# Kernel tuning notes

Measured on AMD Instinct MI355X. Metric: run time of the kernel, lower is better.

Reference implementation:

```python
import jax, jax.numpy as jnp
import numpy as np

B, T, F, H, C = 256, 14, 1024, 1024, 2513


def lstm_step(Wih, Whh, bih, bhh, x, h, c):
    # PyTorch LSTM cell: gate order i, f, g, o
    g = x @ Wih.T + bih + h @ Whh.T + bhh
    i, f, gg, o = jnp.split(g, 4, axis=-1)
    i = jax.nn.sigmoid(i)
    f = jax.nn.sigmoid(f)
    gg = jnp.tanh(gg)
    o = jax.nn.sigmoid(o)
    c = f * c + i * gg
    h = o * jnp.tanh(c)
    return h, c


def setup_inputs() -> dict:
    key = jax.random.key(0)
    ks = jax.random.split(key, 11)
    s = 1.0 / np.sqrt(H)
    u = lambda k, shape: jax.random.uniform(k, shape, jnp.float32, -s, s)
    return {
        "inputs": jax.random.normal(ks[0], (B, T, F), jnp.float32),
        "roll_Wih": u(ks[1], (4 * H, F)),
        "roll_Whh": u(ks[2], (4 * H, H)),
        "roll_bih": u(ks[3], (4 * H,)),
        "roll_bhh": u(ks[4], (4 * H,)),
        "unroll_Wih": u(ks[5], (4 * H, F)),
        "unroll_Whh": u(ks[6], (4 * H, H)),
        "unroll_bih": u(ks[7], (4 * H,)),
        "unroll_bhh": u(ks[8], (4 * H,)),
        "cls_W": u(ks[9], (C, H)),
        "cls_b": u(ks[10], (C,)),
    }


def reference(inputs, roll_Wih, roll_Whh, roll_bih, roll_bhh,
              unroll_Wih, unroll_Whh, unroll_bih, unroll_bhh, cls_W, cls_b):
    x_t = jnp.transpose(inputs, (1, 0, 2))  # [T, B, F]

    # Rolling LSTM: scan over time, keep hidden/cell at every step
    h0 = jnp.zeros((B, H), inputs.dtype)
    c0 = jnp.zeros((B, H), inputs.dtype)

    def roll(carry, xt):
        h, c = carry
        h, c = lstm_step(roll_Wih, roll_Whh, roll_bih, roll_bhh, xt, h, c)
        return (h, c), (h, c)

    _, (hs, cs) = jax.lax.scan(roll, (h0, c0), x_t)  # each [T, B, H]

    # Unrolling LSTM: for each t, feed inputs[t] repeated (T - t + 1) times,
    # starting from (hs[t], cs[t]). Vectorized over t: run T+1 steps for all
    # branches with constant per-branch input x_t[t], then pick step (T - t).
    def unroll(carry, _):
        h, c = carry  # [T, B, H]
        h, c = lstm_step(unroll_Wih, unroll_Whh, unroll_bih, unroll_bhh, x_t, h, c)
        return (h, c), h

    _, h_all = jax.lax.scan(unroll, (hs, cs), None, length=T + 1)  # [T+1, T, B, H]
    t_idx = jnp.arange(T)
    h_n = h_all[T - t_idx, t_idx]  # [T, B, H], last output of each branch

    x = jnp.transpose(h_n, (1, 0, 2))  # [B, T, H]
    y = x @ cls_W.T + cls_b  # [B, T, C]
    return y
```

## Files before the change

### kernel.cpp

```cpp
#include <hip/hip_runtime.h>

#define DEVFN __device__ __forceinline__

typedef __bf16 bf16x8 __attribute__((ext_vector_type(8)));
typedef float floatx4 __attribute__((ext_vector_type(4)));
typedef unsigned short us4 __attribute__((ext_vector_type(4)));


DEVFN unsigned short f2bf(float x) {
    union { float f; unsigned u; } v; v.f = x;
    v.u += 0x7FFFu + ((v.u >> 16) & 1u);
    return (unsigned short)(v.u >> 16);
}

DEVFN float bf2f(unsigned short s) {
    union { unsigned u; float f; } v; v.u = ((unsigned)s) << 16; return v.f;
}

DEVFN float sigm(float x) { return 1.f / (1.f + __expf(-x)); }
DEVFN float tanh_fast(float x) { float t = __expf(2.f * x); return 1.f - 2.f / (t + 1.f); }

DEVFN void gload_lds16(const unsigned short* g, unsigned short* l) {
    __builtin_amdgcn_global_load_lds(
        (__attribute__((address_space(1))) unsigned int*)g,
        (__attribute__((address_space(3))) unsigned int*)l, 16, 0, 0);
}

#define CFENCE asm volatile("" ::: "memory")


__global__ __launch_bounds__(256) void transpose_bt(const float* __restrict__ in,
                                                    unsigned short* __restrict__ out) {
    int idx = blockIdx.x * 256 + threadIdx.x;
    int k4 = (idx & 255) << 2;
    int row = idx >> 8;
    int t = row >> 8, b = row & 255;
    float4 v = *(const float4*)(in + (size_t)(b * 14 + t) * 1024 + k4);
    us4 o = {f2bf(v.x), f2bf(v.y), f2bf(v.z), f2bf(v.w)};
    *(us4*)(out + (size_t)row * 1024 + k4) = o;
}

__global__ __launch_bounds__(256) void conv_w4(const float* __restrict__ s0, const float* __restrict__ s1,
                                               const float* __restrict__ s2, const float* __restrict__ s3,
                                               unsigned short* __restrict__ d0, unsigned short* __restrict__ d1,
                                               unsigned short* __restrict__ d2, unsigned short* __restrict__ d3) {
    int t = blockIdx.x * 256 + threadIdx.x;
    int which = t >> 20;
    int off = (t & 1048575) << 2;
    const float* s = (which == 0) ? s0 : (which == 1) ? s1 : (which == 2) ? s2 : s3;
    unsigned short* d = (which == 0) ? d0 : (which == 1) ? d1 : (which == 2) ? d2 : d3;
    float4 v = *(const float4*)(s + off);
    us4 o = {f2bf(v.x), f2bf(v.y), f2bf(v.z), f2bf(v.w)};
    *(us4*)(d + off) = o;
}

__global__ __launch_bounds__(256) void conv_cls(const float* __restrict__ in,
                                                unsigned short* __restrict__ out) {
    int t = blockIdx.x * 256 + threadIdx.x;
    int off = t << 2;
    us4 o = {0, 0, 0, 0};
    if (off < 2573312) {
        float4 v = *(const float4*)(in + off);
        o = (us4){f2bf(v.x), f2bf(v.y), f2bf(v.z), f2bf(v.w)};
    }
    *(us4*)(out + off) = o;
}

__global__ __launch_bounds__(256) void bias_interleave(const float* __restrict__ a,
                                                       const float* __restrict__ b,
                                                       float* __restrict__ o4, int n) {
    int i = blockIdx.x * 256 + threadIdx.x;
    if (i < n) {
        int g = i >> 10, h = i & 1023;
        o4[h * 4 + g] = a[i] + b[i];
    }
}

template <int MODE, int NH>
__global__ __launch_bounds__(256, 2)
void lstm_big(const unsigned short* __restrict__ A1,
              const unsigned short* __restrict__ W1,
              const unsigned short* __restrict__ W2,
              const unsigned short* __restrict__ pre4b,
              const float* __restrict__ bias4a,
              const float* __restrict__ bias4b,
              const float* __restrict__ c_in,
              float* __restrict__ c_out,
              unsigned short* __restrict__ h_out,
              unsigned short* __restrict__ h_alt, int retire_t,
              unsigned short* __restrict__ g1,
              unsigned short* __restrict__ g2,
              const float* __restrict__ clsb,
              float* __restrict__ outp, int gx) {
    constexpr int BROWS = 4 * NH;
    constexpr int FN = BROWS / 32;
    constexpr int BISS = BROWS / 64;
    constexpr int LOADS = 2 + BISS;
    constexpr int ASH = 4096;
    constexpr int BSH = BROWS * 32;
    constexpr int HH = NH / 32;

    __shared__ __align__(16) unsigned short lds[3][ASH + BSH];

    const int tid = threadIdx.x;
    const int b = blockIdx.x;
    int bx, by;
    if (MODE == 2) {
        int id = ((b & 7) * ((int)gridDim.x >> 3)) + (b >> 3);
        bx = id % gx; by = id / gx;
    } else if (MODE == 4) {
        bx = ((b & 7) << 1) + ((b >> 3) & 1) + (((b >> 4) & 1) << 4);
        by = b >> 5;
    } else if (NH == 64) {
        bx = ((b & 7) << 1) + ((b >> 3) & 1);
        by = b >> 4;
    } else {
        bx = ((b & 7) << 2) + ((b >> 3) & 3);
        by = b >> 5;
    }
    const int m0 = by * 128;
    const int n0h = (MODE == 4) ? (bx & 15) * 64 : bx * NH;
    const int n0c = bx * BROWS;
    const int lane = tid & 63;
    const int wv = tid >> 6;
    const int wm = wv >> 1, wn = wv & 1;
    const int r16 = lane & 15;
    const int kg = lane >> 4;

    const unsigned short* Ws = (MODE == 4 && (bx >> 4)) ? W2 : W1;

    auto stage = [&](int u, int buf) {
        const int ko = u * 32;
#pragma unroll
        for (int is = 0; is < 2; ++is) {
            int c = is * 256 + tid;
            int row = c >> 2, kq = c & 3;
            int kqg = kq ^ ((row >> 1) & 3);
            gload_lds16(A1 + (size_t)(m0 + row) * 1024 + ko + kqg * 8, &lds[buf][c * 8]);
        }
#pragma unroll
        for (int is = 0; is < BISS; ++is) {
            int c = is * 256 + tid;
            int row = c >> 2, kq = c & 3;
            int kqg = kq ^ ((row >> 1) & 3);
            int wr;
            if (MODE == 2) wr = n0c + row;
            else wr = ((row >> 4) & 3) * 1024 + n0h + ((row >> 6) << 4) + (row & 15);
            gload_lds16(Ws + (size_t)wr * 1024 + ko + kqg * 8, &lds[buf][ASH + c * 8]);
        }
    };

    floatx4 acc[4][FN];
#pragma unroll
    for (int i = 0; i < 4; ++i)
#pragma unroll
        for (int j = 0; j < FN; ++j) acc[i][j] = {0.f, 0.f, 0.f, 0.f};

    stage(0, 0);
    stage(1, 1);
    stage(2, 2);
    asm volatile("s_waitcnt vmcnt(%0)" :: "n"(2 * LOADS) : "memory");
    __builtin_amdgcn_s_barrier();
    CFENCE;

    int cur = 0;
    for (int u = 0; u < 32; ++u) {
        bf16x8 a[4], bfr[FN];
#pragma unroll
        for (int i = 0; i < 4; ++i) {
            int row = wm * 64 + i * 16 + r16;
            a[i] = *(const bf16x8*)&lds[cur][row * 32 + (kg ^ ((row >> 1) & 3)) * 8];
        }
#pragma unroll
        for (int j = 0; j < FN; ++j) {
            int row = wn * (BROWS / 2) + j * 16 + r16;
            bfr[j] = *(const bf16x8*)&lds[cur][ASH + row * 32 + (kg ^ ((row >> 1) & 3)) * 8];
        }
        __builtin_amdgcn_s_setprio(1);
#pragma unroll
        for (int i = 0; i < 4; ++i)
#pragma unroll
            for (int j = 0; j < FN; ++j)
                acc[i][j] = __builtin_amdgcn_mfma_f32_16x16x32_bf16(a[i], bfr[j], acc[i][j], 0, 0, 0);
        __builtin_amdgcn_s_setprio(0);

        if (u < 31) {
            __builtin_amdgcn_s_barrier();
            if (u < 29) {
                stage(u + 3, cur);
                asm volatile("s_waitcnt vmcnt(%0)" :: "n"(2 * LOADS) : "memory");
            } else if (u == 29) {
                asm volatile("s_waitcnt vmcnt(%0)" :: "n"(LOADS) : "memory");
            } else {
                asm volatile("s_waitcnt vmcnt(0)" ::: "memory");
            }
            __builtin_amdgcn_s_barrier();
            CFENCE;
        }
        cur = (cur == 2) ? 0 : cur + 1;
    }

    if (MODE == 2) {
#pragma unroll
        for (int i = 0; i < 4; ++i)
#pragma unroll
            for (int j = 0; j < FN; ++j)
#pragma unroll
                for (int rg = 0; rg < 4; ++rg) {
                    int m = m0 + wm * 64 + i * 16 + kg * 4 + rg;
                    int gn = n0c + wn * (BROWS / 2) + j * 16 + r16;
                    if (gn < 2513) {
                        int bb = m & 255, tt = m >> 8;
                        __builtin_nontemporal_store(acc[i][j][rg] + clsb[gn],
                                                    outp + (size_t)(bb * 14 + tt) * 2513 + gn);
                    }
                }
        return;
    }

    if (MODE == 4) {
        const int half = bx >> 4;
        unsigned short* gsel = half ? g2 : g1;
        const float* bsel = half ? bias4b : bias4a;
        const bool cell0 = (half == 1) && (by < 2);
#pragma unroll
        for (int hh = 0; hh < HH; ++hh) {
            const int h = n0h + wn * (NH / 2) + hh * 16 + r16;
            float4 bv = *(const float4*)(bsel + (size_t)h * 4);
#pragma unroll
            for (int i = 0; i < 4; ++i)
#pragma unroll
                for (int rg = 0; rg < 4; ++rg) {
                    int m = m0 + wm * 64 + i * 16 + kg * 4 + rg;
                    size_t mh = (size_t)m * 1024 + h;
                    float gi_ = acc[i][hh * 4 + 0][rg] + bv.x;
                    float gf_ = acc[i][hh * 4 + 1][rg] + bv.y;
                    float gg_ = acc[i][hh * 4 + 2][rg] + bv.z;
                    float go_ = acc[i][hh * 4 + 3][rg] + bv.w;
                    if (cell0) {
                        float iv = sigm(gi_), ov = sigm(go_);
                        float gv = tanh_fast(gg_);
                        float cn = iv * gv;
                        float hn = ov * tanh_fast(cn);
                        c_out[mh] = cn;
                        h_out[mh] = f2bf(hn);
                    } else {
                        us4 o = {f2bf(gi_), f2bf(gf_), f2bf(gg_), f2bf(go_)};
                        *(us4*)(gsel + mh * 4) = o;
                    }
                }
        }
        return;
    }

    unsigned short* hw = h_out;
    if ((m0 >> 8) == retire_t) hw = h_alt;

#pragma unroll
    for (int hh = 0; hh < HH; ++hh) {
        const int h = n0h + wn * (NH / 2) + hh * 16 + r16;
#pragma unroll
        for (int i = 0; i < 4; ++i)
#pragma unroll
            for (int rg = 0; rg < 4; ++rg) {
                int m = m0 + wm * 64 + i * 16 + kg * 4 + rg;
                size_t mh = (size_t)m * 1024 + h;
                us4 pv = *(const us4*)(pre4b + mh * 4);
                float gi_ = acc[i][hh * 4 + 0][rg] + bf2f(pv.x);
                float gf_ = acc[i][hh * 4 + 1][rg] + bf2f(pv.y);
                float gg_ = acc[i][hh * 4 + 2][rg] + bf2f(pv.z);
                float go_ = acc[i][hh * 4 + 3][rg] + bf2f(pv.w);
                float co = c_in[mh];
                float iv = sigm(gi_), fv = sigm(gf_);
                float gv = tanh_fast(gg_), ov = sigm(go_);
                float cn = fv * co + iv * gv;
                float hn = ov * tanh_fast(cn);
                c_out[mh] = cn;
                hw[mh] = f2bf(hn);
            }
    }
}

__global__ __launch_bounds__(256)
void lstm_small(const unsigned short* __restrict__ A1, const unsigned short* __restrict__ W1,
                const unsigned short* __restrict__ pre4b,
                const float* __restrict__ c_in,
                float* __restrict__ c_out,
                unsigned short* __restrict__ h_out,
                unsigned short* __restrict__ h_alt, int retire_t) {
    constexpr int ATILE = 32 * 64;
    constexpr int LOADS = 5;

    __shared__ __align__(16) unsigned short lds[4][ATILE + 8192];

    const int tid = threadIdx.x;
    const int b = blockIdx.x;
    const int bx = ((b & 7) << 2) + ((b >> 3) & 3);
    const int by = b >> 5;
    const int m0 = by * 32;
    const int n0 = bx * 32;
    const int lane = tid & 63;
    const int wv = tid >> 6;
    const int wm = wv >> 1, wn = wv & 1;
    const int r16 = lane & 15;
    const int kg = lane >> 4;

    auto stage = [&](int kt, int buf) {
        const int ko = kt * 64;
        {
            int c = tid;
            int row = c >> 3, kq = c & 7, kqg = kq ^ (row & 7);
            gload_lds16(A1 + (size_t)(m0 + row) * 1024 + ko + kqg * 8, &lds[buf][c * 8]);
        }
#pragma unroll
        for (int is = 0; is < 4; ++is) {
            int c = is * 256 + tid;
            int row = c >> 3, kq = c & 7, kqg = kq ^ (row & 7);
            int wr = ((row >> 4) & 3) * 1024 + n0 + ((row >> 6) << 4) + (row & 15);
            gload_lds16(W1 + (size_t)wr * 1024 + ko + kqg * 8, &lds[buf][ATILE + c * 8]);
        }
    };

    floatx4 acc[4];
#pragma unroll
    for (int j = 0; j < 4; ++j) acc[j] = {0.f, 0.f, 0.f, 0.f};

    stage(0, 0);
    stage(1, 1);
    stage(2, 2);
    asm volatile("s_waitcnt vmcnt(%0)" :: "n"(2 * LOADS) : "memory");
    __builtin_amdgcn_s_barrier();
    CFENCE;

#pragma unroll 4
    for (int u = 0; u < 16; ++u) {
        const int cur = u & 3;
#pragma unroll
        for (int kk = 0; kk < 2; ++kk) {
            bf16x8 a, bfr[4];
            const int kqg = kk * 4 + kg;
            {
                int row = wm * 16 + r16;
                a = *(const bf16x8*)&lds[cur][row * 64 + (kqg ^ (row & 7)) * 8];
            }
#pragma unroll
            for (int j = 0; j < 4; ++j) {
                int row = wn * 64 + j * 16 + r16;
                bfr[j] = *(const bf16x8*)&lds[cur][ATILE + row * 64 + (kqg ^ (row & 7)) * 8];
            }
#pragma unroll
            for (int j = 0; j < 4; ++j)
                acc[j] = __builtin_amdgcn_mfma_f32_16x16x32_bf16(a, bfr[j], acc[j], 0, 0, 0);
        }
        if (u < 15) {
            __builtin_amdgcn_s_barrier();
            if (u < 13) {
                stage(u + 3, (u + 3) & 3);
                asm volatile("s_waitcnt vmcnt(%0)" :: "n"(2 * LOADS) : "memory");
            } else if (u == 13) {
                asm volatile("s_waitcnt vmcnt(%0)" :: "n"(LOADS) : "memory");
            } else {
                asm volatile("s_waitcnt vmcnt(0)" ::: "memory");
            }
            __builtin_amdgcn_s_barrier();
            CFENCE;
        }
    }

    const int h = n0 + wn * 16 + r16;
    unsigned short* hw = h_out;
    if ((m0 >> 8) == retire_t) hw = h_alt;

#pragma unroll
    for (int rg = 0; rg < 4; ++rg) {
        int m = m0 + wm * 16 + kg * 4 + rg;
        size_t mh = (size_t)m * 1024 + h;
        us4 pv = *(const us4*)(pre4b + mh * 4);
        float gi_ = acc[0][rg] + bf2f(pv.x);
        float gf_ = acc[1][rg] + bf2f(pv.y);
        float gg_ = acc[2][rg] + bf2f(pv.z);
        float go_ = acc[3][rg] + bf2f(pv.w);
        float co = c_in[mh];
        float iv = sigm(gi_), fv = sigm(gf_);
        float gv = tanh_fast(gg_), ov = sigm(go_);
        float cn = fv * co + iv * gv;
        float hn = ov * tanh_fast(cn);
        c_out[mh] = cn;
        hw[mh] = f2bf(hn);
    }
}


extern "C" void kernel_launch(void* const* d_in, const int* in_sizes, int n_in,
                              void* d_out, int out_size, void* d_ws, size_t ws_size,
                              hipStream_t stream) {
    (void)in_sizes; (void)n_in; (void)out_size; (void)ws_size;
    const float* inputs   = (const float*)d_in[0];
    const float* roll_Wih = (const float*)d_in[1];
    const float* roll_Whh = (const float*)d_in[2];
    const float* roll_bih = (const float*)d_in[3];
    const float* roll_bhh = (const float*)d_in[4];
    const float* un_Wih   = (const float*)d_in[5];
    const float* un_Whh   = (const float*)d_in[6];
    const float* un_bih   = (const float*)d_in[7];
    const float* un_bhh   = (const float*)d_in[8];
    const float* cls_Wf   = (const float*)d_in[9];
    const float* cls_b    = (const float*)d_in[10];
    float* out = (float*)d_out;

    char* ws = (char*)d_ws;
    size_t off = 0;
    auto alloc = [&](size_t bytes) -> char* {
        char* p = ws + off;
        off += (bytes + 255) & ~(size_t)255;
        return p;
    };
    unsigned short* xt   = (unsigned short*)alloc(3584ull * 1024 * 2);
    unsigned short* rWih = (unsigned short*)alloc(4096ull * 1024 * 2);
    unsigned short* rWhh = (unsigned short*)alloc(4096ull * 1024 * 2);
    unsigned short* uWih = (unsigned short*)alloc(4096ull * 1024 * 2);
    unsigned short* uWhh = (unsigned short*)alloc(4096ull * 1024 * 2);
    unsigned short* cWp  = (unsigned short*)alloc(2560ull * 1024 * 2);
    float* rbias4 = (float*)alloc(1024 * 4 * 4);
    float* ubias4 = (float*)alloc(1024 * 4 * 4);
    unsigned short* XpreB  = (unsigned short*)alloc(3584ull * 4096 * 2);
    unsigned short* XrollB = (unsigned short*)alloc(3584ull * 4096 * 2);
    float* uc     = (float*)alloc(3584ull * 1024 * 4);
    unsigned short* hb0    = (unsigned short*)alloc(3584ull * 1024 * 2);
    unsigned short* hb1    = (unsigned short*)alloc(3584ull * 1024 * 2);
    unsigned short* hfinal = (unsigned short*)alloc(3584ull * 1024 * 2);

    const size_t SF = 256 * 1024;

    transpose_bt<<<3584, 256, 0, stream>>>(inputs, xt);
    conv_w4<<<16384, 256, 0, stream>>>(roll_Wih, roll_Whh, un_Wih, un_Whh,
                                       rWih, rWhh, uWih, uWhh);
    conv_cls<<<2560, 256, 0, stream>>>(cls_Wf, cWp);
    bias_interleave<<<16, 256, 0, stream>>>(roll_bih, roll_bhh, rbias4, 4096);
    bias_interleave<<<16, 256, 0, stream>>>(un_bih, un_bhh, ubias4, 4096);

    lstm_big<4, 64><<<896, 256, 0, stream>>>(
        xt, uWih, rWih, nullptr, ubias4, rbias4,
        nullptr, uc, hb0, nullptr, -1, XpreB, XrollB, nullptr, nullptr, 32);

    for (int t = 1; t < 14; ++t) {
        lstm_small<<<256, 256, 0, stream>>>(
            hb0 + (size_t)(t - 1) * SF, rWhh,
            XrollB + (size_t)t * SF * 4,
            uc + (size_t)(t - 1) * SF, uc + (size_t)t * SF,
            hb0 + (size_t)t * SF, nullptr, -1);
    }

    for (int s = 0; s <= 14; ++s) {
        int nb = (15 - s < 14) ? (15 - s) : 14;
        int M = nb * 256;
        const unsigned short* hsrc = (s & 1) ? hb1 : hb0;
        unsigned short* hdst = (s & 1) ? hb0 : hb1;
        int rt = (s >= 1) ? (14 - s) : -1;
        if (M >= 2304) {
            lstm_big<1, 64><<<M / 8, 256, 0, stream>>>(
                hsrc, uWhh, nullptr, XpreB, nullptr, nullptr,
                uc, uc, hdst, hfinal, rt, nullptr, nullptr, nullptr, nullptr, 16);
        } else if (M >= 1024) {
            lstm_big<1, 32><<<M / 4, 256, 0, stream>>>(
                hsrc, uWhh, nullptr, XpreB, nullptr, nullptr,
                uc, uc, hdst, hfinal, rt, nullptr, nullptr, nullptr, nullptr, 32);
        } else {
            lstm_small<<<M, 256, 0, stream>>>(
                hsrc, uWhh, XpreB, uc, uc, hdst, hfinal, rt);
        }
    }

    lstm_big<2, 64><<<280, 256, 0, stream>>>(
        hfinal, cWp, nullptr, nullptr, nullptr, nullptr,
        nullptr, nullptr, nullptr, nullptr, -1, nullptr, nullptr, cls_b, out, 10);
}
```

Baseline: 698.1 us.

## Add 256x256-tile 512-thread GEMM kernel for large LSTM and classifier GEMMs

Introduces lstm_mega, a 512-thread (8-wave) kernel computing 256x256 output tiles with BK=64, double-buffered LDS (128KB) and a finer-grained staged load schedule interleaved with MFMA phases. It replaces lstm_big for the input-projection GEMM, the large unrolled recurrent steps and the classifier GEMM, halving block counts and increasing operand reuse per tile. lstm_big is simplified to only the NH=32 recurrent path. The trade-off is a large LDS footprint and register pressure per block, with fewer blocks which may underfill CUs on smaller launches such as the 140-block classifier.

```diff
diff --git a/kernel.cpp b/kernel.cpp
--- a/kernel.cpp
+++ b/kernel.cpp
@@ -76,22 +76,223 @@
     }
 }
 
+template <int MODE>
+__global__ __launch_bounds__(512, 2)
+void lstm_mega(const unsigned short* __restrict__ A1,
+               const unsigned short* __restrict__ W1,
+               const unsigned short* __restrict__ W2,
+               const unsigned short* __restrict__ pre4b,
+               const float* __restrict__ bias4a,
+               const float* __restrict__ bias4b,
+               const float* __restrict__ c_in,
+               float* __restrict__ c_out,
+               unsigned short* __restrict__ h_out,
+               unsigned short* __restrict__ h_alt, int retire_t,
+               unsigned short* __restrict__ g1,
+               unsigned short* __restrict__ g2,
+               const float* __restrict__ clsb,
+               float* __restrict__ outp) {
+    __shared__ __align__(16) unsigned short lds[2][32768];
+
+    const int tid = threadIdx.x;
+    const int b = blockIdx.x;
+    int bx, by;
+    if (MODE == 2) {
+        bx = b % 10; by = b / 10;
+    } else if (MODE == 4) {
+        int sel = (b >> 3) & 3;
+        bx = ((sel & 1) << 4) + ((b & 7) << 1) + (sel >> 1);
+        by = b >> 5;
+    } else {
+        bx = ((b & 7) << 1) + ((b >> 3) & 1);
+        by = b >> 4;
+    }
+    const int m0 = by * 256;
+    const int n0h = (MODE == 4) ? (bx & 15) * 64 : bx * 64;
+    const int n0c = bx * 256;
+    const int lane = tid & 63;
+    const int wv = tid >> 6;
+    const int wm = wv >> 2, wn = wv & 3;
+    const int r16 = lane & 15;
+    const int kg = lane >> 4;
+
+    const unsigned short* Ws = (MODE == 4 && (bx >> 4)) ? W2 : W1;
+
+    auto st = [&](int t, int s) {
+        if (t >= 16) return;
+        const int ko = t * 64;
+        if (s < 4) {
+            int rb = s * 64 + (tid >> 3);
+            int kq = tid & 7;
+            int kqg = kq ^ (rb & 7);
+            int wr;
+            if (MODE == 2) wr = n0c + rb;
+            else wr = ((rb >> 4) & 3) * 1024 + n0h + ((rb >> 6) << 4) + (rb & 15);
+            gload_lds16(Ws + (size_t)wr * 1024 + ko + kqg * 8,
+                        &lds[t & 1][16384 + s * 4096 + tid * 8]);
+        } else {
+            int q = s - 4;
+            int lr = tid >> 3;
+            int rlog = ((lr >> 5) << 7) + q * 32 + (lr & 31);
+            int kq = tid & 7;
+            int kqg = kq ^ (lr & 7);
+            gload_lds16(A1 + (size_t)(m0 + rlog) * 1024 + ko + kqg * 8,
+                        &lds[t & 1][q * 4096 + tid * 8]);
+        }
+    };
+
+    floatx4 acc[8][4];
+#pragma unroll
+    for (int i = 0; i < 8; ++i)
+#pragma unroll
+        for (int j = 0; j < 4; ++j) acc[i][j] = {0.f, 0.f, 0.f, 0.f};
+
+#pragma unroll
+    for (int s = 0; s < 8; ++s) st(0, s);
+#pragma unroll
+    for (int s = 0; s < 6; ++s) st(1, s);
+    asm volatile("s_waitcnt vmcnt(6)" ::: "memory");
+    __builtin_amdgcn_s_barrier();
+    CFENCE;
+
+    for (int v = 0; v < 8; ++v) {
+        const int te = 2 * v;
+        bf16x8 bfr[4][2];
+#pragma unroll
+        for (int p = 0; p < 8; ++p) {
+            const int q = p & 3;
+            const int buf = p >> 2;
+            if (p == 0) {
+                asm volatile("s_waitcnt vmcnt(6)" ::: "memory");
+            } else if (p == 4) {
+                if (v == 7) asm volatile("s_waitcnt vmcnt(0)" ::: "memory");
+                else        asm volatile("s_waitcnt vmcnt(6)" ::: "memory");
+            }
+            if (q == 0) {
+#pragma unroll
+                for (int j = 0; j < 4; ++j)
+#pragma unroll
+                    for (int kk = 0; kk < 2; ++kk) {
+                        int rb = wn * 64 + j * 16 + r16;
+                        bfr[j][kk] = *(const bf16x8*)&lds[buf][16384 + rb * 64 +
+                                         (((kk << 2) + kg) ^ (rb & 7)) * 8];
+                    }
+            }
+            bf16x8 a[2][2];
+#pragma unroll
+            for (int i = 0; i < 2; ++i)
+#pragma unroll
+                for (int kk = 0; kk < 2; ++kk) {
+                    int ra = q * 64 + wm * 32 + i * 16 + r16;
+                    a[i][kk] = *(const bf16x8*)&lds[buf][ra * 64 +
+                                   (((kk << 2) + kg) ^ (ra & 7)) * 8];
+                }
+            {
+                int tt = (p == 0) ? te + 1 : (p <= 4 ? te + 2 : te + 3);
+                int s0 = (p == 0 || p == 4) ? 6 : ((p == 1 || p == 5) ? 0 :
+                         ((p == 2 || p == 6) ? 2 : 4));
+                st(tt, s0);
+                st(tt, s0 + 1);
+            }
+            __builtin_amdgcn_s_barrier();
+            CFENCE;
+            __builtin_amdgcn_s_setprio(1);
+#pragma unroll
+            for (int i = 0; i < 2; ++i)
+#pragma unroll
+                for (int j = 0; j < 4; ++j)
+#pragma unroll
+                    for (int kk = 0; kk < 2; ++kk)
+                        acc[q * 2 + i][j] = __builtin_amdgcn_mfma_f32_16x16x32_bf16(
+                            a[i][kk], bfr[j][kk], acc[q * 2 + i][j], 0, 0, 0);
+            __builtin_amdgcn_s_setprio(0);
+            __builtin_amdgcn_s_barrier();
+            CFENCE;
+        }
+    }
+
+    if (MODE == 2) {
+#pragma unroll
+        for (int i = 0; i < 8; ++i)
+#pragma unroll
+            for (int j = 0; j < 4; ++j)
+#pragma unroll
+                for (int rg = 0; rg < 4; ++rg) {
+                    int m = m0 + wm * 128 + i * 16 + kg * 4 + rg;
+                    int gn = n0c + wn * 64 + j * 16 + r16;
+                    if (gn < 2513) {
+                        int bb = m & 255, tt = m >> 8;
+                        __builtin_nontemporal_store(acc[i][j][rg] + clsb[gn],
+                                                    outp + (size_t)(bb * 14 + tt) * 2513 + gn);
+                    }
+                }
+        return;
+    }
+
+    const int h = n0h + wn * 16 + r16;
+
+    if (MODE == 4) {
+        const int half = bx >> 4;
+        unsigned short* gsel = half ? g2 : g1;
+        const float* bsel = half ? bias4b : bias4a;
+        const bool cell0 = (half == 1) && (by == 0);
+        float4 bv = *(const float4*)(bsel + (size_t)h * 4);
+#pragma unroll
+        for (int i = 0; i < 8; ++i)
+#pragma unroll
+            for (int rg = 0; rg < 4; ++rg) {
+                int m = m0 + wm * 128 + i * 16 + kg * 4 + rg;
+                size_t mh = (size_t)m * 1024 + h;
+                float gi_ = acc[i][0][rg] + bv.x;
+                float gf_ = acc[i][1][rg] + bv.y;
+                float gg_ = acc[i][2][rg] + bv.z;
+                float go_ = acc[i][3][rg] + bv.w;
+                if (cell0) {
+                    float iv = sigm(gi_), ov = sigm(go_);
+                    float gv = tanh_fast(gg_);
+                    float cn = iv * gv;
+                    float hn = ov * tanh_fast(cn);
+                    c_out[mh] = cn;
+                    h_out[mh] = f2bf(hn);
+                } else {
+                    us4 o = {f2bf(gi_), f2bf(gf_), f2bf(gg_), f2bf(go_)};
+                    *(us4*)(gsel + mh * 4) = o;
+                }
+            }
+        return;
+    }
+
+    unsigned short* hw = (by == retire_t) ? h_alt : h_out;
+#pragma unroll
+    for (int i = 0; i < 8; ++i)
+#pragma unroll
+        for (int rg = 0; rg < 4; ++rg) {
+            int m = m0 + wm * 128 + i * 16 + kg * 4 + rg;
+            size_t mh = (size_t)m * 1024 + h;
+            us4 pv = *(const us4*)(pre4b + mh * 4);
+            float gi_ = acc[i][0][rg] + bf2f(pv.x);
+            float gf_ = acc[i][1][rg] + bf2f(pv.y);
+            float gg_ = acc[i][2][rg] + bf2f(pv.z);
+            float go_ = acc[i][3][rg] + bf2f(pv.w);
+            float co = c_in[mh];
+            float iv = sigm(gi_), fv = sigm(gf_);
+            float gv = tanh_fast(gg_), ov = sigm(go_);
+            float cn = fv * co + iv * gv;
+            float hn = ov * tanh_fast(cn);
+            c_out[mh] = cn;
+            hw[mh] = f2bf(hn);
+        }
+}
+
 template <int MODE, int NH>
 __global__ __launch_bounds__(256, 2)
 void lstm_big(const unsigned short* __restrict__ A1,
               const unsigned short* __restrict__ W1,
-              const unsigned short* __restrict__ W2,
               const unsigned short* __restrict__ pre4b,
-              const float* __restrict__ bias4a,
-              const float* __restrict__ bias4b,
               const float* __restrict__ c_in,
               float* __restrict__ c_out,
               unsigned short* __restrict__ h_out,
-              unsigned short* __restrict__ h_alt, int retire_t,
-              unsigned short* __restrict__ g1,
-              unsigned short* __restrict__ g2,
-              const float* __restrict__ clsb,
-              float* __restrict__ outp, int gx) {
+              unsigned short* __restrict__ h_alt, int retire_t, int gx) {
     constexpr int BROWS = 4 * NH;
     constexpr int FN = BROWS / 32;
     constexpr int BISS = BROWS / 64;
@@ -104,30 +305,16 @@
 
     const int tid = threadIdx.x;
     const int b = blockIdx.x;
-    int bx, by;
-    if (MODE == 2) {
-        int id = ((b & 7) * ((int)gridDim.x >> 3)) + (b >> 3);
-        bx = id % gx; by = id / gx;
-    } else if (MODE == 4) {
-        bx = ((b & 7) << 1) + ((b >> 3) & 1) + (((b >> 4) & 1) << 4);
-        by = b >> 5;
-    } else if (NH == 64) {
-        bx = ((b & 7) << 1) + ((b >> 3) & 1);
-        by = b >> 4;
-    } else {
-        bx = ((b & 7) << 2) + ((b >> 3) & 3);
-        by = b >> 5;
-    }
+    const int bx = ((b & 7) << 2) + ((b >> 3) & 3);
+    const int by = b >> 5;
     const int m0 = by * 128;
-    const int n0h = (MODE == 4) ? (bx & 15) * 64 : bx * NH;
-    const int n0c = bx * BROWS;
+    const int n0h = bx * NH;
     const int lane = tid & 63;
     const int wv = tid >> 6;
     const int wm = wv >> 1, wn = wv & 1;
     const int r16 = lane & 15;
     const int kg = lane >> 4;
-
-    const unsigned short* Ws = (MODE == 4 && (bx >> 4)) ? W2 : W1;
+    (void)gx;
 
     auto stage = [&](int u, int buf) {
         const int ko = u * 32;
@@ -143,10 +330,8 @@
             int c = is * 256 + tid;
             int row = c >> 2, kq = c & 3;
             int kqg = kq ^ ((row >> 1) & 3);
-            int wr;
-            if (MODE == 2) wr = n0c + row;
-            else wr = ((row >> 4) & 3) * 1024 + n0h + ((row >> 6) << 4) + (row & 15);
-            gload_lds16(Ws + (size_t)wr * 1024 + ko + kqg * 8, &lds[buf][ASH + c * 8]);
+            int wr = ((row >> 4) & 3) * 1024 + n0h + ((row >> 6) << 4) + (row & 15);
+            gload_lds16(W1 + (size_t)wr * 1024 + ko + kqg * 8, &lds[buf][ASH + c * 8]);
         }
     };
 
@@ -200,62 +385,7 @@
         cur = (cur == 2) ? 0 : cur + 1;
     }
 
-    if (MODE == 2) {
-#pragma unroll
-        for (int i = 0; i < 4; ++i)
-#pragma unroll
-            for (int j = 0; j < FN; ++j)
-#pragma unroll
-                for (int rg = 0; rg < 4; ++rg) {
-                    int m = m0 + wm * 64 + i * 16 + kg * 4 + rg;
-                    int gn = n0c + wn * (BROWS / 2) + j * 16 + r16;
-                    if (gn < 2513) {
-                        int bb = m & 255, tt = m >> 8;
-                        __builtin_nontemporal_store(acc[i][j][rg] + clsb[gn],
-                                                    outp + (size_t)(bb * 14 + tt) * 2513 + gn);
-                    }
-                }
-        return;
-    }
-
-    if (MODE == 4) {
-        const int half = bx >> 4;
-        unsigned short* gsel = half ? g2 : g1;
-        const float* bsel = half ? bias4b : bias4a;
-        const bool cell0 = (half == 1) && (by < 2);
-#pragma unroll
-        for (int hh = 0; hh < HH; ++hh) {
-            const int h = n0h + wn * (NH / 2) + hh * 16 + r16;
-            float4 bv = *(const float4*)(bsel + (size_t)h * 4);
-#pragma unroll
-            for (int i = 0; i < 4; ++i)
-#pragma unroll
-                for (int rg = 0; rg < 4; ++rg) {
-                    int m = m0 + wm * 64 + i * 16 + kg * 4 + rg;
-                    size_t mh = (size_t)m * 1024 + h;
-                    float gi_ = acc[i][hh * 4 + 0][rg] + bv.x;
-                    float gf_ = acc[i][hh * 4 + 1][rg] + bv.y;
-                    float gg_ = acc[i][hh * 4 + 2][rg] + bv.z;
-                    float go_ = acc[i][hh * 4 + 3][rg] + bv.w;
-                    if (cell0) {
-                        float iv = sigm(gi_), ov = sigm(go_);
-                        float gv = tanh_fast(gg_);
-                        float cn = iv * gv;
-                        float hn = ov * tanh_fast(cn);
-                        c_out[mh] = cn;
-                        h_out[mh] = f2bf(hn);
-                    } else {
-                        us4 o = {f2bf(gi_), f2bf(gf_), f2bf(gg_), f2bf(go_)};
-                        *(us4*)(gsel + mh * 4) = o;
-                    }
-                }
-        }
-        return;
-    }
-
-    unsigned short* hw = h_out;
-    if ((m0 >> 8) == retire_t) hw = h_alt;
-
+    unsigned short* hw = ((m0 >> 8) == retire_t) ? h_alt : h_out;
 #pragma unroll
     for (int hh = 0; hh < HH; ++hh) {
         const int h = n0h + wn * (NH / 2) + hh * 16 + r16;
@@ -368,8 +498,7 @@
     }
 
     const int h = n0 + wn * 16 + r16;
-    unsigned short* hw = h_out;
-    if ((m0 >> 8) == retire_t) hw = h_alt;
+    unsigned short* hw = ((m0 >> 8) == retire_t) ? h_alt : h_out;
 
 #pragma unroll
     for (int rg = 0; rg < 4; ++rg) {
@@ -439,9 +568,9 @@
     bias_interleave<<<16, 256, 0, stream>>>(roll_bih, roll_bhh, rbias4, 4096);
     bias_interleave<<<16, 256, 0, stream>>>(un_bih, un_bhh, ubias4, 4096);
 
-    lstm_big<4, 64><<<896, 256, 0, stream>>>(
+    lstm_mega<4><<<448, 512, 0, stream>>>(
         xt, uWih, rWih, nullptr, ubias4, rbias4,
-        nullptr, uc, hb0, nullptr, -1, XpreB, XrollB, nullptr, nullptr, 32);
+        nullptr, uc, hb0, nullptr, -1, XpreB, XrollB, nullptr, nullptr);
 
     for (int t = 1; t < 14; ++t) {
         lstm_small<<<256, 256, 0, stream>>>(
@@ -458,20 +587,19 @@
         unsigned short* hdst = (s & 1) ? hb0 : hb1;
         int rt = (s >= 1) ? (14 - s) : -1;
         if (M >= 2304) {
-            lstm_big<1, 64><<<M / 8, 256, 0, stream>>>(
+            lstm_mega<1><<<nb * 16, 512, 0, stream>>>(
                 hsrc, uWhh, nullptr, XpreB, nullptr, nullptr,
-                uc, uc, hdst, hfinal, rt, nullptr, nullptr, nullptr, nullptr, 16);
+                uc, uc, hdst, hfinal, rt, nullptr, nullptr, nullptr, nullptr);
         } else if (M >= 1024) {
             lstm_big<1, 32><<<M / 4, 256, 0, stream>>>(
-                hsrc, uWhh, nullptr, XpreB, nullptr, nullptr,
-                uc, uc, hdst, hfinal, rt, nullptr, nullptr, nullptr, nullptr, 32);
+                hsrc, uWhh, XpreB, uc, uc, hdst, hfinal, rt, 32);
         } else {
             lstm_small<<<M, 256, 0, stream>>>(
                 hsrc, uWhh, XpreB, uc, uc, hdst, hfinal, rt);
         }
     }
 
-    lstm_big<2, 64><<<280, 256, 0, stream>>>(
+    lstm_mega<2><<<140, 512, 0, stream>>>(
         hfinal, cWp, nullptr, nullptr, nullptr, nullptr,
-        nullptr, nullptr, nullptr, nullptr, -1, nullptr, nullptr, cls_b, out, 10);
-}
+        nullptr, nullptr, nullptr, nullptr, -1, nullptr, nullptr, cls_b, out);
+}
```

After: 684.6 us. About the same (-1.9%).
